# Performance work log

Hardware: AMD Instinct MI355X
Metric: run time of the kernel (lower is better)

Reference implementation:

```python
import jax, jax.numpy as jnp
import numpy as np
from jax import lax

BITS = 8
STRIDE = 1
PADDING = 1
SCALE = 2.0 ** (BITS - 1)  # fixed-point scale 2^(bits-1)


def setup_inputs() -> dict:
    key = jax.random.key(0)
    k1, k2, k3 = jax.random.split(key, 3)
    x = jax.random.normal(k1, (32, 128, 56, 56), dtype=jnp.float32)
    W = jax.random.normal(k2, (256, 128, 3, 3), dtype=jnp.float32)
    b = jax.random.normal(k3, (256,), dtype=jnp.float32)
    return {"x": x, "W": W, "b": b}


def reference(x, W, b):
    # to_fix_point: round(v * 2^(bits-1)); torch keeps long ints, but all
    # arithmetic in forward promotes back to float, so float round is exact here.
    w_q = jnp.round(W * SCALE)
    b_q = jnp.round(b * SCALE)
    # calConv: out[i,j] = sum(patch * w_q) / 2^(bits-1) + b_q
    # (square 3x3 kernel makes the original's transposed patch indexing a standard conv)
    out = lax.conv_general_dilated(
        x, w_q,
        window_strides=(STRIDE, STRIDE),
        padding=[(PADDING, PADDING), (PADDING, PADDING)],
        dimension_numbers=("NCHW", "OIHW", "NCHW"),
    )
    return out / SCALE + b_q[None, :, None, None]
```

## Files before the change

### kernel.cpp

```cpp
#include <hip/hip_runtime.h>

typedef _Float16 half8 __attribute__((ext_vector_type(8)));
typedef float floatx4 __attribute__((ext_vector_type(4)));

#define IMG   3136
#define PIMG  3364
#define XP_ELEMS (32 * 58 * 58 * 128)
#define WQ_ELEMS (9 * 256 * 128)

#define AS1 __attribute__((address_space(1)))
#define AS3 __attribute__((address_space(3)))

__global__ __launch_bounds__(256) void pad_x_kernel(const float* __restrict__ x,
                                                    _Float16* __restrict__ xp) {
    const int hh = blockIdx.x;
    const int n  = blockIdx.y;
    const int t  = threadIdx.x;
    _Float16* rowbase = xp + ((long)(n * 58 + hh) * 58) * 128;

    if (hh == 0 || hh == 57) {
        #pragma unroll
        for (int i = 0; i < 4; ++i) {
            int idx = i * 256 + t;
            if (idx < 928) *(half8*)(rowbase + idx * 8) = (half8)(_Float16)0.0f;
        }
        return;
    }

    __shared__ _Float16 tile[128 * 57];
    const int h = hh - 1;

    #pragma unroll
    for (int p = 0; p < 7; ++p) {
        int idx = p * 256 + t;
        int c   = idx / 14;
        int w4  = (idx % 14) * 4;
        const float4 v = *(const float4*)(x + ((long)(n * 128 + c) * 56 + h) * 56 + w4);
        _Float16* d = tile + c * 57 + w4;
        d[0] = (_Float16)v.x; d[1] = (_Float16)v.y;
        d[2] = (_Float16)v.z; d[3] = (_Float16)v.w;
    }
    __syncthreads();

    #pragma unroll
    for (int p = 0; p < 4; ++p) {
        int idx = p * 256 + t;
        if (idx < 896) {
            int ww = idx >> 4;
            int c0 = (idx & 15) * 8;
            half8 v;
            #pragma unroll
            for (int j = 0; j < 8; ++j) v[j] = tile[(c0 + j) * 57 + ww];
            *(half8*)(rowbase + (ww + 1) * 128 + c0) = v;
        }
    }
    if (t < 32) {
        int ww = (t >> 4) ? 57 : 0;
        int c0 = (t & 15) * 8;
        *(half8*)(rowbase + ww * 128 + c0) = (half8)(_Float16)0.0f;
    }
}

__global__ void quant_w_kernel(const float* __restrict__ W, _Float16* __restrict__ wq) {
    int t = blockIdx.x * 256 + threadIdx.x;
    int c  = t & 127;
    int k  = (t >> 7) & 255;
    int rs = t >> 15;
    wq[t] = (_Float16)rintf(W[(k * 128 + c) * 9 + rs] * 128.0f);
}

__global__ __launch_bounds__(256) void conv_mfma_kernel(
    const _Float16* __restrict__ xp, const _Float16* __restrict__ wq,
    const float* __restrict__ b, float* __restrict__ out)
{
    __shared__ __align__(16) _Float16 smem[16384];

    const int tid = threadIdx.x;
    const int l   = tid & 63;
    const int wv  = tid >> 6;
    const int wm  = wv & 1;
    const int wn  = wv >> 1;
    const int bx  = blockIdx.x;
    const int by  = blockIdx.y;

    const int lrow = l >> 2;
    const int lcol = ((l & 3) ^ ((l >> 3) & 3)) * 8;

    const int aoff0 = (by * 128 + wv * 16 + lrow) * 128 + lcol;
    const int aoff1 = aoff0 + 64 * 128;

    const int pix0 = bx * 128 + wv * 16 + lrow;
    const int pix1 = pix0 + 64;
    const int n0 = pix0 / IMG, hw0 = pix0 % IMG;
    const int n1 = pix1 / IMG, hw1 = pix1 % IMG;
    const int pb0 = (n0 * PIMG + (hw0 / 56) * 58 + (hw0 % 56)) * 128 + lcol;
    const int pb1 = (n1 * PIMG + (hw1 / 56) * 58 + (hw1 % 56)) * 128 + lcol;

    const int stageoff = wv * 512;

    floatx4 acc[4][4] = {};

    auto issue = [&](int t, int pbuf) {
        const int rs = t >> 2;
        const int cc = t & 3;
        const int r  = (rs * 11) >> 5;
        const int s2 = rs - r * 3;
        const _Float16* wg = wq + rs * (256 * 128);
        const _Float16* xg = xp + (r * 58 + s2) * 128;
        const int co = cc * 32;
        _Float16* A = smem + pbuf * 8192 + stageoff;
        _Float16* B = smem + pbuf * 8192 + 4096 + stageoff;
        __builtin_amdgcn_global_load_lds((AS1 void*)(wg + aoff0 + co), (AS3 void*)A,          16, 0, 0);
        __builtin_amdgcn_global_load_lds((AS1 void*)(wg + aoff1 + co), (AS3 void*)(A + 2048), 16, 0, 0);
        __builtin_amdgcn_global_load_lds((AS1 void*)(xg + pb0  + co), (AS3 void*)B,          16, 0, 0);
        __builtin_amdgcn_global_load_lds((AS1 void*)(xg + pb1  + co), (AS3 void*)(B + 2048), 16, 0, 0);
    };

    const int ar = wm * 64 + (l & 15);
    const int br = wn * 64 + (l & 15);
    const int kq = ((l >> 4) ^ ((l >> 1) & 3)) * 8;

    auto compute = [&](int pbuf) {
        const _Float16* As = smem + pbuf * 8192;
        const _Float16* Bs = As + 4096;
        half8 af[4], bf[4];
        #pragma unroll
        for (int mi = 0; mi < 4; ++mi)
            af[mi] = *(const half8*)(As + (ar + mi * 16) * 32 + kq);
        #pragma unroll
        for (int ni = 0; ni < 4; ++ni)
            bf[ni] = *(const half8*)(Bs + (br + ni * 16) * 32 + kq);
        #pragma unroll
        for (int mi = 0; mi < 4; ++mi)
            #pragma unroll
            for (int ni = 0; ni < 4; ++ni)
                acc[mi][ni] = __builtin_amdgcn_mfma_f32_16x16x32_f16(af[mi], bf[ni], acc[mi][ni], 0, 0, 0);
    };

    issue(0, 0);
    #pragma unroll 2
    for (int s = 0; s < 35; ++s) {
        issue(s + 1, (s + 1) & 1);
        asm volatile("s_waitcnt vmcnt(4)" ::: "memory");
        asm volatile("s_barrier" ::: "memory");
        compute(s & 1);
        asm volatile("s_barrier" ::: "memory");
    }
    asm volatile("s_waitcnt vmcnt(0)" ::: "memory");
    asm volatile("s_barrier" ::: "memory");
    compute(1);

    #pragma unroll
    for (int mi = 0; mi < 4; ++mi) {
        const int kb = by * 128 + wm * 64 + mi * 16 + (l >> 4) * 4;
        #pragma unroll
        for (int rg = 0; rg < 4; ++rg) {
            const int k = kb + rg;
            const float bq = rintf(b[k] * 128.0f);
            #pragma unroll
            for (int ni = 0; ni < 4; ++ni) {
                const int pix = bx * 128 + wn * 64 + ni * 16 + (l & 15);
                const int n  = pix / IMG;
                const int pr = pix - n * IMG;
                out[((long)n * 256 + k) * IMG + pr] = acc[mi][ni][rg] * (1.0f / 128.0f) + bq;
            }
        }
    }
}

__global__ void conv_fallback_kernel(const float* __restrict__ x, const float* __restrict__ W,
                                     const float* __restrict__ b, float* __restrict__ out)
{
    __shared__ float wsm[1152];
    const int k = blockIdx.y;
    for (int i = threadIdx.x; i < 1152; i += 256)
        wsm[i] = rintf(W[k * 1152 + i] * 128.0f);
    __syncthreads();
    const int pix = blockIdx.x * 256 + threadIdx.x;
    const int n = pix / IMG, hw = pix % IMG;
    const int h = hw / 56, w = hw % 56;
    float acc = 0.0f;
    for (int c = 0; c < 128; ++c) {
        const float* xr = x + ((n * 128 + c) * 56) * 56;
        const float* wr = wsm + c * 9;
        #pragma unroll
        for (int r = 0; r < 3; ++r) {
            const int hh = h + r - 1;
            if ((unsigned)hh >= 56u) continue;
            #pragma unroll
            for (int s = 0; s < 3; ++s) {
                const int ww = w + s - 1;
                if ((unsigned)ww >= 56u) continue;
                acc += xr[hh * 56 + ww] * wr[r * 3 + s];
            }
        }
    }
    out[((long)n * 256 + k) * IMG + hw] = acc * (1.0f / 128.0f) + rintf(b[k] * 128.0f);
}

extern "C" void kernel_launch(void* const* d_in, const int* in_sizes, int n_in,
                              void* d_out, int out_size, void* d_ws, size_t ws_size,
                              hipStream_t stream) {
    const float* x = (const float*)d_in[0];
    const float* W = (const float*)d_in[1];
    const float* b = (const float*)d_in[2];
    float* out = (float*)d_out;

    const size_t need = (size_t)XP_ELEMS * 2 + (size_t)WQ_ELEMS * 2;
    if (ws_size >= need) {
        _Float16* xp = (_Float16*)d_ws;
        _Float16* wq = xp + XP_ELEMS;
        pad_x_kernel<<<dim3(58, 32), 256, 0, stream>>>(x, xp);
        quant_w_kernel<<<WQ_ELEMS / 256, 256, 0, stream>>>(W, wq);
        conv_mfma_kernel<<<dim3(784, 2), 256, 0, stream>>>(xp, wq, b, out);
    } else {
        conv_fallback_kernel<<<dim3(392, 256), 256, 0, stream>>>(x, W, b, out);
    }
}
```

Before: 214.5 us.

## Enlarge conv block tile to cover all 256 output channels

Each block now computes all 256 output channels for its 128 pixels instead of splitting the channels across two blocks. The input tile is loaded from global memory once rather than twice, and each wave holds an 8x4 grid of MFMA accumulators. The cost is double the accumulator registers (128 floats per lane), more LDS per block (48KB), and half as many blocks (784), which can lower occupancy and latency hiding.

```diff
diff --git a/kernel.cpp b/kernel.cpp
--- a/kernel.cpp
+++ b/kernel.cpp
@@ -73,7 +73,7 @@
     const _Float16* __restrict__ xp, const _Float16* __restrict__ wq,
     const float* __restrict__ b, float* __restrict__ out)
 {
-    __shared__ __align__(16) _Float16 smem[16384];
+    __shared__ __align__(16) _Float16 smem[24576];
 
     const int tid = threadIdx.x;
     const int l   = tid & 63;
@@ -81,67 +81,71 @@
     const int wm  = wv & 1;
     const int wn  = wv >> 1;
     const int bx  = blockIdx.x;
-    const int by  = blockIdx.y;
 
     const int lrow = l >> 2;
-    const int lcol = ((l & 3) ^ ((l >> 3) & 3)) * 8;
-
-    const int aoff0 = (by * 128 + wv * 16 + lrow) * 128 + lcol;
-    const int aoff1 = aoff0 + 64 * 128;
-
-    const int pix0 = bx * 128 + wv * 16 + lrow;
-    const int pix1 = pix0 + 64;
-    const int n0 = pix0 / IMG, hw0 = pix0 % IMG;
-    const int n1 = pix1 / IMG, hw1 = pix1 % IMG;
-    const int pb0 = (n0 * PIMG + (hw0 / 56) * 58 + (hw0 % 56)) * 128 + lcol;
-    const int pb1 = (n1 * PIMG + (hw1 / 56) * 58 + (hw1 % 56)) * 128 + lcol;
-
-    const int stageoff = wv * 512;
-
-    floatx4 acc[4][4] = {};
+    const int lch  = ((l & 3) ^ ((l >> 3) & 3)) * 8;
+
+    int aoff[4];
+    #pragma unroll
+    for (int i = 0; i < 4; ++i)
+        aoff[i] = (i * 64 + wv * 16 + lrow) * 128 + lch;
+
+    int pb[2];
+    #pragma unroll
+    for (int j = 0; j < 2; ++j) {
+        const int pix = bx * 128 + j * 64 + wv * 16 + lrow;
+        const int n  = pix / IMG, hw = pix % IMG;
+        pb[j] = (n * PIMG + (hw / 56) * 58 + (hw % 56)) * 128 + lch;
+    }
+
+    const int stA = wv * 512;
+
+    floatx4 acc[8][4] = {};
 
     auto issue = [&](int t, int pbuf) {
         const int rs = t >> 2;
         const int cc = t & 3;
         const int r  = (rs * 11) >> 5;
         const int s2 = rs - r * 3;
-        const _Float16* wg = wq + rs * (256 * 128);
-        const _Float16* xg = xp + (r * 58 + s2) * 128;
-        const int co = cc * 32;
-        _Float16* A = smem + pbuf * 8192 + stageoff;
-        _Float16* B = smem + pbuf * 8192 + 4096 + stageoff;
-        __builtin_amdgcn_global_load_lds((AS1 void*)(wg + aoff0 + co), (AS3 void*)A,          16, 0, 0);
-        __builtin_amdgcn_global_load_lds((AS1 void*)(wg + aoff1 + co), (AS3 void*)(A + 2048), 16, 0, 0);
-        __builtin_amdgcn_global_load_lds((AS1 void*)(xg + pb0  + co), (AS3 void*)B,          16, 0, 0);
-        __builtin_amdgcn_global_load_lds((AS1 void*)(xg + pb1  + co), (AS3 void*)(B + 2048), 16, 0, 0);
+        const _Float16* wg = wq + rs * (256 * 128) + cc * 32;
+        const _Float16* xg = xp + (r * 58 + s2) * 128 + cc * 32;
+        _Float16* A = smem + pbuf * 12288;
+        _Float16* B = A + 8192;
+        #pragma unroll
+        for (int i = 0; i < 4; ++i)
+            __builtin_amdgcn_global_load_lds((AS1 void*)(wg + aoff[i]),
+                                             (AS3 void*)(A + i * 2048 + stA), 16, 0, 0);
+        #pragma unroll
+        for (int j = 0; j < 2; ++j)
+            __builtin_amdgcn_global_load_lds((AS1 void*)(xg + pb[j]),
+                                             (AS3 void*)(B + j * 2048 + stA), 16, 0, 0);
     };
 
-    const int ar = wm * 64 + (l & 15);
+    const int ar = wm * 128 + (l & 15);
     const int br = wn * 64 + (l & 15);
     const int kq = ((l >> 4) ^ ((l >> 1) & 3)) * 8;
 
     auto compute = [&](int pbuf) {
-        const _Float16* As = smem + pbuf * 8192;
-        const _Float16* Bs = As + 4096;
-        half8 af[4], bf[4];
-        #pragma unroll
-        for (int mi = 0; mi < 4; ++mi)
-            af[mi] = *(const half8*)(As + (ar + mi * 16) * 32 + kq);
+        const _Float16* As = smem + pbuf * 12288;
+        const _Float16* Bs = As + 8192;
+        half8 bf[4];
         #pragma unroll
         for (int ni = 0; ni < 4; ++ni)
             bf[ni] = *(const half8*)(Bs + (br + ni * 16) * 32 + kq);
         #pragma unroll
-        for (int mi = 0; mi < 4; ++mi)
+        for (int mi = 0; mi < 8; ++mi) {
+            const half8 af = *(const half8*)(As + (ar + mi * 16) * 32 + kq);
             #pragma unroll
             for (int ni = 0; ni < 4; ++ni)
-                acc[mi][ni] = __builtin_amdgcn_mfma_f32_16x16x32_f16(af[mi], bf[ni], acc[mi][ni], 0, 0, 0);
+                acc[mi][ni] = __builtin_amdgcn_mfma_f32_16x16x32_f16(af, bf[ni], acc[mi][ni], 0, 0, 0);
+        }
     };
 
     issue(0, 0);
     #pragma unroll 2
     for (int s = 0; s < 35; ++s) {
         issue(s + 1, (s + 1) & 1);
-        asm volatile("s_waitcnt vmcnt(4)" ::: "memory");
+        asm volatile("s_waitcnt vmcnt(6)" ::: "memory");
         asm volatile("s_barrier" ::: "memory");
         compute(s & 1);
         asm volatile("s_barrier" ::: "memory");
@@ -151,8 +155,8 @@
     compute(1);
 
     #pragma unroll
-    for (int mi = 0; mi < 4; ++mi) {
-        const int kb = by * 128 + wm * 64 + mi * 16 + (l >> 4) * 4;
+    for (int mi = 0; mi < 8; ++mi) {
+        const int kb = wm * 128 + mi * 16 + (l >> 4) * 4;
         #pragma unroll
         for (int rg = 0; rg < 4; ++rg) {
             const int k = kb + rg;
@@ -212,7 +216,7 @@
         _Float16* wq = xp + XP_ELEMS;
         pad_x_kernel<<<dim3(58, 32), 256, 0, stream>>>(x, xp);
         quant_w_kernel<<<WQ_ELEMS / 256, 256, 0, stream>>>(W, wq);
-        conv_mfma_kernel<<<dim3(784, 2), 256, 0, stream>>>(xp, wq, b, out);
+        conv_mfma_kernel<<<dim3(784), 256, 0, stream>>>(xp, wq, b, out);
     } else {
         conv_fallback_kernel<<<dim3(392, 256), 256, 0, stream>>>(x, W, b, out);
     }
```

Result: faster. 206.9 us (-3.5%).
